# Optimization experiments

Hardware: AMD Instinct MI355X
Metric: run time of the kernel (lower is better)

## Reference

```python
import jax, jax.numpy as jnp
import numpy as np

T = 5          # temporal_window_size
B = 512        # batch (graphs per timestep)
NA = 16        # num_agents (nodes per graph)
S = 64         # num_belief_states
A = 16         # action_dim
HID = 64       # hidden_dim per head
H = 4          # num_attn_heads
FD = HID * H   # 256, feature_dim
LAT = 128      # latent_dim
N = B * NA     # total nodes per timestep
FIN = S + A    # node feature dim
NEG_SLOPE = 0.2


def _edge_index():
    i, j = np.meshgrid(np.arange(NA), np.arange(NA), indexing='ij')
    m = i != j
    src_l, dst_l = i[m], j[m]                      # 240 intra-clique edges
    off = (np.arange(B) * NA)[:, None]
    src = (src_l[None] + off).ravel()
    dst = (dst_l[None] + off).ravel()
    loops = np.arange(N)                           # PyG GATConv add_self_loops=True
    src = np.concatenate([src, loops])
    dst = np.concatenate([dst, loops])
    return jnp.asarray(np.stack([src, dst]), dtype=jnp.int64)


def setup_inputs() -> dict:
    key = jax.random.key(0)
    ks = jax.random.split(key, 24)
    xav = lambda k, shp: jax.random.normal(k, shp, jnp.float32) * np.float32(np.sqrt(2.0 / (shp[0] + shp[-1])))
    return {
        'signals': jax.random.normal(ks[0], (T, B, S), jnp.float32),
        'neighbor_actions': jax.random.normal(ks[1], (T, B, NA * A), jnp.float32),
        'lin_w0': xav(ks[2], (FD, FIN)),
        'att_src0': xav(ks[3], (H, HID)),
        'att_dst0': xav(ks[4], (H, HID)),
        'bias0': jnp.zeros((FD,), jnp.float32),
        'lin_w1': xav(ks[5], (FD, FD)),
        'att_src1': xav(ks[6], (H, HID)),
        'att_dst1': xav(ks[7], (H, HID)),
        'bias1': jnp.zeros((FD,), jnp.float32),
        'in_proj_w': xav(ks[8], (3 * FD, FD)),
        'in_proj_b': jnp.zeros((3 * FD,), jnp.float32),
        'out_proj_w': xav(ks[9], (FD, FD)),
        'out_proj_b': jnp.zeros((FD,), jnp.float32),
        'w_mean': xav(ks[10], (LAT, FD)),
        'b_mean': jnp.zeros((LAT,), jnp.float32),
        'w_logvar': xav(ks[11], (LAT, FD)),
        'b_logvar': jnp.zeros((LAT,), jnp.float32),
        'w_belief': xav(ks[12], (S, FD)),
        'b_belief': jnp.zeros((S,), jnp.float32),
        'edge_index': _edge_index(),
    }


def _segment_softmax(e, seg, num_segments):
    # e: [E, T, H]; softmax over edges sharing the same target node.
    m = jax.ops.segment_max(e, seg, num_segments=num_segments)
    e = jnp.exp(e - m[seg])
    s = jax.ops.segment_sum(e, seg, num_segments=num_segments)
    return e / s[seg]


def _gat(x, src, dst, w, a_src, a_dst, b):
    # x: [N, T, Fin] -> [N, T, H*HID]   (PyG GATConv, concat heads)
    xl = jnp.einsum('ntf,of->nto', x, w).reshape(N, T, H, HID)
    e_src = jnp.einsum('nthc,hc->nth', xl, a_src)[src]   # [E, T, H]
    e_dst = jnp.einsum('nthc,hc->nth', xl, a_dst)[dst]
    e = jax.nn.leaky_relu(e_src + e_dst, NEG_SLOPE)
    alpha = _segment_softmax(e, dst, N)                  # per-target softmax
    out = jax.ops.segment_sum(alpha[..., None] * xl[src], dst, num_segments=N)
    return out.reshape(N, T, FD) + b


def reference(signals, neighbor_actions, lin_w0, att_src0, att_dst0, bias0,
              lin_w1, att_src1, att_dst1, bias1, in_proj_w, in_proj_b,
              out_proj_w, out_proj_b, w_mean, b_mean, w_logvar, b_logvar,
              w_belief, b_belief, edge_index):
    # --- _construct_graph (vectorized over time window + batch) ---
    acts = neighbor_actions.reshape(T, B, NA, A)
    beliefs = jnp.zeros((T, B, NA, S), signals.dtype).at[:, :, 0, :].set(signals)
    nodes = jnp.concatenate([beliefs, acts], -1).reshape(T, N, FIN)
    nodes = jnp.transpose(nodes, (1, 0, 2))              # [N, T, FIN]
    src, dst = edge_index[0], edge_index[1]
    x = jax.nn.relu(_gat(nodes, src, dst, lin_w0, att_src0, att_dst0, bias0))
    x = jax.nn.relu(_gat(x, src, dst, lin_w1, att_src1, att_dst1, bias1))
    # --- ego-node sequence: nodes 0, NA, 2*NA, ... ---
    seq = x[::NA]                                        # [B, T, FD]
    # --- temporal MultiheadAttention (batch_first, eval) ---
    qkv = seq @ in_proj_w.T + in_proj_b
    q, k, v = jnp.split(qkv, 3, axis=-1)
    dh = FD // H
    q = q.reshape(B, T, H, dh); k = k.reshape(B, T, H, dh); v = v.reshape(B, T, H, dh)
    scores = jnp.einsum('bqhd,bkhd->bhqk', q, k) / jnp.sqrt(jnp.asarray(dh, seq.dtype))
    # torch float attn_mask is ADDITIVE: mask[i,j]=1 if j<=i else 0
    mask = (jnp.arange(T)[:, None] >= jnp.arange(T)[None, :]).astype(seq.dtype)
    attn = jax.nn.softmax(scores + mask[None, None], axis=-1)
    ctx = jnp.einsum('bhqk,bkhd->bqhd', attn, v).reshape(B, T, FD)
    ctx = ctx @ out_proj_w.T + out_proj_b
    feat = ctx[:, -1]                                    # [B, FD]
    # --- heads ---
    mean = feat @ w_mean.T + b_mean
    logvar = feat @ w_logvar.T + b_logvar
    belief = jax.nn.softmax(feat @ w_belief.T + b_belief, axis=-1)
    return (mean, logvar, belief)
```

## Files before the change

### kernel.cpp

```cpp
#include <hip/hip_runtime.h>
#include <hip/hip_bf16.h>


__device__ __forceinline__ float wave_sum64(float v) {
    #pragma unroll
    for (int off = 32; off > 0; off >>= 1) v += __shfl_xor(v, off, 64);
    return v;
}
__device__ __forceinline__ float wave_max64(float v) {
    #pragma unroll
    for (int off = 32; off > 0; off >>= 1) v = fmaxf(v, __shfl_xor(v, off, 64));
    return v;
}

__global__ __launch_bounds__(256) void k_pre(
    const float* __restrict__ w0, const float* __restrict__ w1,
    const float* __restrict__ wip, const float* __restrict__ wop,
    const float* __restrict__ wm, const float* __restrict__ wlv,
    const float* __restrict__ wb,
    const float* __restrict__ as0, const float* __restrict__ ad0,
    const float* __restrict__ as1, const float* __restrict__ ad1,
    float* __restrict__ tws,
    float* __restrict__ u1, float* __restrict__ ud1,
    float* __restrict__ pa0, float* __restrict__ pd0)
{
    const int tid = threadIdx.x;
    if (blockIdx.x < 1680) {
        int i = blockIdx.x * 256 + tid;
        float v;
        if (i < 16384) {
            int k = i >> 8, n = i & 255;
            v = w0[n * 80 + k];
        } else if (i < 20480) {
            int j = i - 16384; int k = j >> 8, n = j & 255;
            v = w0[n * 80 + 64 + k];
        } else if (i < 86016) {
            int j = i - 20480; int k = j >> 8, n = j & 255;
            v = w1[n * 256 + k];
        } else if (i < 282624) {
            int j = i - 86016; int k = j / 768, n = j - k * 768;
            v = wip[n * 256 + k];
        } else if (i < 348160) {
            int j = i - 282624; int k = j >> 8, n = j & 255;
            v = wop[n * 256 + k];
        } else {
            int j = i - 348160; int k = j / 320, o = j - k * 320;
            if (o < 128)      v = wm[o * 256 + k];
            else if (o < 256) v = wlv[(o - 128) * 256 + k];
            else              v = wb[(o - 256) * 256 + k];
        }
        tws[i] = v;
        return;
    }
    for (int q = 0; q < 4; q++) {
        int idx = q * 256 + tid;
        int h = idx >> 8, k = idx & 255;
        float su = 0.f, sd = 0.f;
        for (int c = 0; c < 64; c++) {
            float wv = w1[(h * 64 + c) * 256 + k];
            su = fmaf(as1[h * 64 + c], wv, su);
            sd = fmaf(ad1[h * 64 + c], wv, sd);
        }
        u1[idx] = su; ud1[idx] = sd;
    }
    if (tid < 64) {
        int h = tid >> 4, k = tid & 15;
        float su = 0.f, sd = 0.f;
        for (int c = 0; c < 64; c++) {
            float wv = w0[(h * 64 + c) * 80 + 64 + k];
            su = fmaf(as0[h * 64 + c], wv, su);
            sd = fmaf(ad0[h * 64 + c], wv, sd);
        }
        pa0[tid] = su; pd0[tid] = sd;
    }
}

__global__ __launch_bounds__(256, 4) void k_gat(
    const float* __restrict__ sig,
    const float* __restrict__ nact,
    const float* __restrict__ W0sT,
    const float* __restrict__ W0aT,
    const float* __restrict__ W1T,
    const float* __restrict__ u1g, const float* __restrict__ ud1g,
    const float* __restrict__ pa0g, const float* __restrict__ pd0g,
    const float* __restrict__ as0, const float* __restrict__ ad0,
    const float* __restrict__ b0, const float* __restrict__ b1,
    float* __restrict__ seqf)
{
    __shared__ __align__(16) char smem[37120];
    float* actL    = (float*)(smem + 0);
    float* sigL    = (float*)(smem + 1024);
    float* u1L     = (float*)(smem + 1280);
    float* ud1L    = (float*)(smem + 5440);
    float* pa0L    = (float*)(smem + 9600);
    float* pd0L    = (float*)(smem + 9856);
    float* es0w    = (float*)(smem + 10112);
    float* ed0w    = (float*)(smem + 10368);
    float* espL    = (float*)(smem + 10624);
    float* es1L    = (float*)(smem + 11648);
    float* edpL    = (float*)(smem + 11904);
    float* alpha1L = (float*)(smem + 11968);
    float* a0L     = (float*)(smem + 12224);
    float* zL      = (float*)(smem + 16320);
    float* x1L     = (float*)(smem + 20480);

    const int tid = threadIdx.x;
    const int bg = blockIdx.x;
    const int b = bg / 5, g = bg - b * 5;
    const int n = tid, w = tid >> 6, lane = tid & 63;

    if (tid < 64) sigL[tid] = sig[(g * 512 + b) * 64 + tid];
    actL[tid] = nact[(g * 512 + b) * 256 + tid];
    #pragma unroll
    for (int q = 0; q < 4; q++) {
        int idx = q * 256 + tid;
        int h = idx >> 8, k = idx & 255;
        u1L[h * 260 + k] = u1g[idx];
        ud1L[h * 260 + k] = ud1g[idx];
    }
    if (tid >= 64 && tid < 128) {
        pa0L[tid - 64] = pa0g[tid - 64];
        pd0L[tid - 64] = pd0g[tid - 64];
    }
    __syncthreads();

    float S = 0.f;
    {
        const float4* sig4 = (const float4*)sigL;
        #pragma unroll
        for (int i = 0; i < 4; i++) {
            float wv[16];
            #pragma unroll
            for (int j = 0; j < 16; j++)
                wv[j] = W0sT[(i * 16 + j) * 256 + n];
            #pragma unroll
            for (int q = 0; q < 4; q++) {
                float4 sv = sig4[i * 4 + q];
                S = fmaf(wv[q * 4 + 0], sv.x, S);
                S = fmaf(wv[q * 4 + 1], sv.y, S);
                S = fmaf(wv[q * 4 + 2], sv.z, S);
                S = fmaf(wv[q * 4 + 3], sv.w, S);
            }
        }
    }
    const float sS = wave_sum64(S * as0[n]);
    const float dS = wave_sum64(S * ad0[n]);

    if (lane < 16) {
        const int m = lane;
        float su = (m == 0) ? sS : 0.f;
        float sd = (m == 0) ? dS : 0.f;
        const float4* act4 = (const float4*)(actL + m * 16);
        const float4* pa4  = (const float4*)(pa0L + w * 16);
        const float4* pd4  = (const float4*)(pd0L + w * 16);
        #pragma unroll
        for (int q = 0; q < 4; q++) {
            float4 av = act4[q], pv = pa4[q], dv = pd4[q];
            su = fmaf(av.x, pv.x, su); su = fmaf(av.y, pv.y, su);
            su = fmaf(av.z, pv.z, su); su = fmaf(av.w, pv.w, su);
            sd = fmaf(av.x, dv.x, sd); sd = fmaf(av.y, dv.y, sd);
            sd = fmaf(av.z, dv.z, sd); sd = fmaf(av.w, dv.w, sd);
        }
        es0w[w * 16 + m] = su;
        ed0w[w * 16 + m] = sd;
    }
    if (lane < 16) {
        const int j = lane;
        float ej = ed0w[w * 16 + j];
        float e[16], m = -1e30f;
        const float4* es4 = (const float4*)(es0w + w * 16);
        #pragma unroll
        for (int s4 = 0; s4 < 4; s4++) {
            float4 ev = es4[s4];
            float x;
            x = ev.x + ej; x = (x >= 0.f) ? x : 0.2f * x; e[s4*4+0] = x; m = fmaxf(m, x);
            x = ev.y + ej; x = (x >= 0.f) ? x : 0.2f * x; e[s4*4+1] = x; m = fmaxf(m, x);
            x = ev.z + ej; x = (x >= 0.f) ? x : 0.2f * x; e[s4*4+2] = x; m = fmaxf(m, x);
            x = ev.w + ej; x = (x >= 0.f) ? x : 0.2f * x; e[s4*4+3] = x; m = fmaxf(m, x);
        }
        float sum = 0.f;
        #pragma unroll
        for (int s = 0; s < 16; s++) { e[s] = __expf(e[s] - m); sum += e[s]; }
        float inv = 1.f / sum;
        float4* a04 = (float4*)(a0L + w * 256 + j * 16);
        #pragma unroll
        for (int s4 = 0; s4 < 4; s4++)
            a04[s4] = make_float4(e[s4 * 4] * inv, e[s4 * 4 + 1] * inv,
                                  e[s4 * 4 + 2] * inv, e[s4 * 4 + 3] * inv);
    }

    float x1r[16];
    {
        float wr[16];
        #pragma unroll
        for (int k = 0; k < 16; k++) wr[k] = W0aT[k * 256 + n];
        const float4* act4 = (const float4*)actL;
        float xl0r[16];
        #pragma unroll
        for (int s = 0; s < 16; s++) {
            float a = 0.f;
            #pragma unroll
            for (int q = 0; q < 4; q++) {
                float4 av = act4[s * 4 + q];
                a = fmaf(av.x, wr[q * 4 + 0], a);
                a = fmaf(av.y, wr[q * 4 + 1], a);
                a = fmaf(av.z, wr[q * 4 + 2], a);
                a = fmaf(av.w, wr[q * 4 + 3], a);
            }
            xl0r[s] = a;
        }
        xl0r[0] += S;
        const float b0v = b0[n];
        const float4* a04 = (const float4*)(a0L + w * 256);
        #pragma unroll
        for (int j = 0; j < 16; j++) {
            float acc = b0v;
            #pragma unroll
            for (int s4 = 0; s4 < 4; s4++) {
                float4 a4 = a04[j * 4 + s4];
                acc = fmaf(a4.x, xl0r[s4 * 4 + 0], acc);
                acc = fmaf(a4.y, xl0r[s4 * 4 + 1], acc);
                acc = fmaf(a4.z, xl0r[s4 * 4 + 2], acc);
                acc = fmaf(a4.w, xl0r[s4 * 4 + 3], acc);
            }
            x1r[j] = fmaxf(acc, 0.f);
            x1L[j * 260 + n] = x1r[j];
        }
    }
    __syncthreads();

    {
        const int m = tid & 15, h = (tid >> 4) & 3, p = tid >> 6;
        const float4* x4p = (const float4*)(x1L + m * 260 + p * 64);
        const float4* u4p = (const float4*)(u1L + h * 260 + p * 64);
        float a = 0.f;
        #pragma unroll
        for (int i = 0; i < 16; i++) {
            float4 xv = x4p[i], uv = u4p[i];
            a = fmaf(xv.x, uv.x, a);
            a = fmaf(xv.y, uv.y, a);
            a = fmaf(xv.z, uv.z, a);
            a = fmaf(xv.w, uv.w, a);
        }
        espL[m * 16 + h * 4 + p] = a;
        if (m == 0) {
            const float4* ud4p = (const float4*)(ud1L + h * 260 + p * 64);
            float ad = 0.f;
            #pragma unroll
            for (int i = 0; i < 16; i++) {
                float4 xv = x4p[i], uv = ud4p[i];
                ad = fmaf(xv.x, uv.x, ad);
                ad = fmaf(xv.y, uv.y, ad);
                ad = fmaf(xv.z, uv.z, ad);
                ad = fmaf(xv.w, uv.w, ad);
            }
            edpL[h * 4 + p] = ad;
        }
    }
    __syncthreads();

    if (w == 0) {
        {
            const int m = lane >> 2, h = lane & 3;
            const float* e = espL + m * 16 + h * 4;
            es1L[m * 4 + h] = e[0] + e[1] + e[2] + e[3];
        }
        if (lane < 4) {
            const int h = lane;
            float ej = edpL[h * 4] + edpL[h * 4 + 1] + edpL[h * 4 + 2] + edpL[h * 4 + 3];
            float e[16], m = -1e30f;
            #pragma unroll
            for (int s = 0; s < 16; s++) {
                float x = es1L[s * 4 + h] + ej;
                x = (x >= 0.f) ? x : 0.2f * x;
                e[s] = x; m = fmaxf(m, x);
            }
            float sum = 0.f;
            #pragma unroll
            for (int s = 0; s < 16; s++) { e[s] = __expf(e[s] - m); sum += e[s]; }
            float inv = 1.f / sum;
            #pragma unroll
            for (int s = 0; s < 16; s++) alpha1L[h * 16 + s] = e[s] * inv;
        }
    }
    __syncthreads();

    {
        const float4* a14 = (const float4*)alpha1L;
        #pragma unroll
        for (int hh = 0; hh < 4; hh++) {
            float zv = 0.f;
            #pragma unroll
            for (int s4 = 0; s4 < 4; s4++) {
                float4 a4 = a14[hh * 4 + s4];
                zv = fmaf(a4.x, x1r[s4 * 4 + 0], zv);
                zv = fmaf(a4.y, x1r[s4 * 4 + 1], zv);
                zv = fmaf(a4.z, x1r[s4 * 4 + 2], zv);
                zv = fmaf(a4.w, x1r[s4 * 4 + 3], zv);
            }
            zL[hh * 260 + n] = zv;
        }
    }
    __syncthreads();

    {
        const float4* zh = (const float4*)(zL + w * 260);
        float acc = b1[n];
        for (int i = 0; i < 16; i++) {
            float wv[16];
            #pragma unroll
            for (int j = 0; j < 16; j++)
                wv[j] = W1T[(i * 16 + j) * 256 + n];
            #pragma unroll
            for (int q = 0; q < 4; q++) {
                float4 z4 = zh[i * 4 + q];
                acc = fmaf(wv[q * 4 + 0], z4.x, acc);
                acc = fmaf(wv[q * 4 + 1], z4.y, acc);
                acc = fmaf(wv[q * 4 + 2], z4.z, acc);
                acc = fmaf(wv[q * 4 + 3], z4.w, acc);
            }
        }
        seqf[bg * 256 + n] = fmaxf(acc, 0.f);
    }
}

__global__ __launch_bounds__(768) void k_stage2(
    const float* __restrict__ seqf,
    const float* __restrict__ wipT,
    const float* __restrict__ bip,
    const float* __restrict__ wopT,
    const float* __restrict__ bop,
    const float* __restrict__ whT,
    const float* __restrict__ bm, const float* __restrict__ blv,
    const float* __restrict__ bb,
    float* __restrict__ out)
{
    __shared__ float sseq[2][5][256];
    __shared__ float kL[2][5][256], vL[2][5][256], qL[2][256];
    __shared__ float ctxL[2][256], featL[2][256];
    __shared__ float beliefL[2][64];
    const int tid = threadIdx.x;
    const int b0 = blockIdx.x * 2;

    {
        float* sflat = &sseq[0][0][0];
        for (int i = tid; i < 2560; i += 768)
            sflat[i] = seqf[b0 * 1280 + i];
    }
    __syncthreads();

    {
        const int kind = tid >> 8, n = tid & 255;
        if (kind == 0) {
            float a0 = 0.f, a1 = 0.f;
            for (int k = 0; k < 256; k++) {
                float wv = wipT[k * 768 + n];
                a0 = fmaf(sseq[0][4][k], wv, a0);
                a1 = fmaf(sseq[1][4][k], wv, a1);
            }
            float bv = bip[n];
            qL[0][n] = a0 + bv; qL[1][n] = a1 + bv;
        } else {
            const float* wcol = wipT + kind * 256 + n;
            float acc[2][5];
            #pragma unroll
            for (int gb = 0; gb < 2; gb++)
                #pragma unroll
                for (int t = 0; t < 5; t++) acc[gb][t] = 0.f;
            for (int k = 0; k < 256; k++) {
                float wv = wcol[k * 768];
                #pragma unroll
                for (int gb = 0; gb < 2; gb++) {
                    #pragma unroll
                    for (int t = 0; t < 5; t++)
                        acc[gb][t] = fmaf(sseq[gb][t][k], wv, acc[gb][t]);
                }
            }
            float bv = bip[kind * 256 + n];
            float* dst = (kind == 1) ? &kL[0][0][0] : &vL[0][0][0];
            #pragma unroll
            for (int gb = 0; gb < 2; gb++)
                #pragma unroll
                for (int t = 0; t < 5; t++)
                    dst[gb * 1280 + t * 256 + n] = acc[gb][t] + bv;
        }
    }
    __syncthreads();

    if (tid < 512) {
        const int gb = tid >> 8, col = tid & 255;
        float q4 = qL[gb][col];
        float sc[5];
        #pragma unroll
        for (int t = 0; t < 5; t++)
            sc[t] = wave_sum64(q4 * kL[gb][t][col]) * 0.125f;
        float m = sc[0];
        #pragma unroll
        for (int t = 1; t < 5; t++) m = fmaxf(m, sc[t]);
        float p[5], sum = 0.f;
        #pragma unroll
        for (int t = 0; t < 5; t++) { p[t] = __expf(sc[t] - m); sum += p[t]; }
        float inv = 1.f / sum, cv = 0.f;
        #pragma unroll
        for (int t = 0; t < 5; t++) cv = fmaf(p[t], vL[gb][t][col], cv);
        ctxL[gb][col] = cv * inv;
    }
    __syncthreads();

    if (tid < 512) {
        const int gb = tid >> 8, n = tid & 255;
        float acc = 0.f;
        for (int k = 0; k < 256; k++)
            acc = fmaf(ctxL[gb][k], wopT[k * 256 + n], acc);
        featL[gb][n] = acc + bop[n];
    }
    __syncthreads();

    if (tid < 640) {
        const int gb = tid / 320, j = tid - gb * 320;
        float acc = 0.f;
        for (int k = 0; k < 256; k++)
            acc = fmaf(featL[gb][k], whT[k * 320 + j], acc);
        if (j < 128) {
            out[(b0 + gb) * 128 + j] = acc + bm[j];
        } else if (j < 256) {
            out[65536 + (b0 + gb) * 128 + (j - 128)] = acc + blv[j - 128];
        } else {
            beliefL[gb][j - 256] = acc + bb[j - 256];
        }
    }
    __syncthreads();

    if (tid < 128) {
        int gb = tid >> 6, lane = tid & 63;
        float lg = beliefL[gb][lane];
        float m = wave_max64(lg);
        float e = __expf(lg - m);
        float s = wave_sum64(e);
        out[131072 + (b0 + gb) * 64 + lane] = e / s;
    }
}

extern "C" void kernel_launch(void* const* d_in, const int* in_sizes, int n_in,
                              void* d_out, int out_size, void* d_ws, size_t ws_size,
                              hipStream_t stream) {
    const float* sig  = (const float*)d_in[0];
    const float* nact = (const float*)d_in[1];
    const float* w0   = (const float*)d_in[2];
    const float* as0  = (const float*)d_in[3];
    const float* ad0  = (const float*)d_in[4];
    const float* b0   = (const float*)d_in[5];
    const float* w1   = (const float*)d_in[6];
    const float* as1  = (const float*)d_in[7];
    const float* ad1  = (const float*)d_in[8];
    const float* b1   = (const float*)d_in[9];
    const float* wip  = (const float*)d_in[10];
    const float* bip  = (const float*)d_in[11];
    const float* wop  = (const float*)d_in[12];
    const float* bop  = (const float*)d_in[13];
    const float* wm   = (const float*)d_in[14];
    const float* bm   = (const float*)d_in[15];
    const float* wlv  = (const float*)d_in[16];
    const float* blv  = (const float*)d_in[17];
    const float* wb   = (const float*)d_in[18];
    const float* bb   = (const float*)d_in[19];

    float* ws    = (float*)d_ws;
    float* seqf  = ws;
    float* tws   = ws + 655360;
    float* W0sT  = tws;
    float* W0aT  = tws + 16384;
    float* W1T   = tws + 20480;
    float* wipT  = tws + 86016;
    float* wopT  = tws + 282624;
    float* whT   = tws + 348160;
    float* u1    = ws + 1085440;
    float* ud1   = ws + 1086464;
    float* pa0   = ws + 1087488;
    float* pd0   = ws + 1087552;

    k_pre   <<<1681, 256, 0, stream>>>(w0, w1, wip, wop, wm, wlv, wb,
                                       as0, ad0, as1, ad1,
                                       tws, u1, ud1, pa0, pd0);
    k_gat   <<<2560, 256, 0, stream>>>(sig, nact, W0sT, W0aT, W1T,
                                       u1, ud1, pa0, pd0, as0, ad0, b0, b1, seqf);
    k_stage2<<<256, 768, 0, stream>>>(seqf, wipT, bip, wopT, bop, whT,
                                      bm, blv, bb, (float*)d_out);
}
```

Before: 199.8 us.

## Coalesce weight transpose reads, drop u1 LDS staging, simplify GAT weight loops

The weight pre-transpose kernel now reads source matrices contiguously and scatters the transposed writes, where before it gathered strided reads and wrote contiguously. The GAT kernel no longer stages u1/ud1 into shared memory and reads them straight from global memory, which shrinks LDS use. The W0s and W1 matvec loops are changed from explicit 16-register prefetch blocks to partially unrolled loops that read weights inline. The launch-bounds occupancy hint is removed, so register allocation is left to the compiler. Possible downsides are uncoalesced writes in k_pre, repeated global/cache reads of u1, and less memory-level parallelism in the matvec loops.

```diff
diff --git a/kernel.cpp b/kernel.cpp
--- a/kernel.cpp
+++ b/kernel.cpp
@@ -20,36 +20,39 @@
     const float* __restrict__ wb,
     const float* __restrict__ as0, const float* __restrict__ ad0,
     const float* __restrict__ as1, const float* __restrict__ ad1,
-    float* __restrict__ tws,
+    float* __restrict__ W0sT, float* __restrict__ W0aT,
+    float* __restrict__ W1T,  float* __restrict__ wipT,
+    float* __restrict__ wopT, float* __restrict__ whT,
     float* __restrict__ u1, float* __restrict__ ud1,
     float* __restrict__ pa0, float* __restrict__ pd0)
 {
     const int tid = threadIdx.x;
     if (blockIdx.x < 1680) {
         int i = blockIdx.x * 256 + tid;
-        float v;
-        if (i < 16384) {
-            int k = i >> 8, n = i & 255;
-            v = w0[n * 80 + k];
-        } else if (i < 20480) {
-            int j = i - 16384; int k = j >> 8, n = j & 255;
-            v = w0[n * 80 + 64 + k];
+        if (i < 20480) {
+            int n = i / 80, k = i - n * 80;
+            float v = w0[i];
+            if (k < 64) W0sT[k * 256 + n] = v;
+            else        W0aT[(k - 64) * 256 + n] = v;
         } else if (i < 86016) {
-            int j = i - 20480; int k = j >> 8, n = j & 255;
-            v = w1[n * 256 + k];
+            int j = i - 20480; int n = j >> 8, k = j & 255;
+            W1T[k * 256 + n] = w1[j];
         } else if (i < 282624) {
-            int j = i - 86016; int k = j / 768, n = j - k * 768;
-            v = wip[n * 256 + k];
+            int j = i - 86016; int n = j >> 8, k = j & 255;
+            wipT[k * 768 + n] = wip[j];
         } else if (i < 348160) {
-            int j = i - 282624; int k = j >> 8, n = j & 255;
-            v = wop[n * 256 + k];
+            int j = i - 282624; int n = j >> 8, k = j & 255;
+            wopT[k * 256 + n] = wop[j];
+        } else if (i < 380928) {
+            int j = i - 348160; int o = j >> 8, k = j & 255;
+            whT[k * 320 + o] = wm[j];
+        } else if (i < 413696) {
+            int j = i - 380928; int o = j >> 8, k = j & 255;
+            whT[k * 320 + 128 + o] = wlv[j];
         } else {
-            int j = i - 348160; int k = j / 320, o = j - k * 320;
-            if (o < 128)      v = wm[o * 256 + k];
-            else if (o < 256) v = wlv[(o - 128) * 256 + k];
-            else              v = wb[(o - 256) * 256 + k];
-        }
-        tws[i] = v;
+            int j = i - 413696; int o = j >> 8, k = j & 255;
+            whT[k * 320 + 256 + o] = wb[j];
+        }
         return;
     }
     for (int q = 0; q < 4; q++) {
@@ -75,7 +78,7 @@
     }
 }
 
-__global__ __launch_bounds__(256, 4) void k_gat(
+__global__ __launch_bounds__(256) void k_gat(
     const float* __restrict__ sig,
     const float* __restrict__ nact,
     const float* __restrict__ W0sT,
@@ -87,22 +90,20 @@
     const float* __restrict__ b0, const float* __restrict__ b1,
     float* __restrict__ seqf)
 {
-    __shared__ __align__(16) char smem[37120];
+    __shared__ __align__(16) char smem[28800];
     float* actL    = (float*)(smem + 0);
     float* sigL    = (float*)(smem + 1024);
-    float* u1L     = (float*)(smem + 1280);
-    float* ud1L    = (float*)(smem + 5440);
-    float* pa0L    = (float*)(smem + 9600);
-    float* pd0L    = (float*)(smem + 9856);
-    float* es0w    = (float*)(smem + 10112);
-    float* ed0w    = (float*)(smem + 10368);
-    float* espL    = (float*)(smem + 10624);
-    float* es1L    = (float*)(smem + 11648);
-    float* edpL    = (float*)(smem + 11904);
-    float* alpha1L = (float*)(smem + 11968);
-    float* a0L     = (float*)(smem + 12224);
-    float* zL      = (float*)(smem + 16320);
-    float* x1L     = (float*)(smem + 20480);
+    float* pa0L    = (float*)(smem + 1280);
+    float* pd0L    = (float*)(smem + 1536);
+    float* es0w    = (float*)(smem + 1792);
+    float* ed0w    = (float*)(smem + 2048);
+    float* espL    = (float*)(smem + 2304);
+    float* es1L    = (float*)(smem + 3328);
+    float* edpL    = (float*)(smem + 3584);
+    float* alpha1L = (float*)(smem + 3648);
+    float* a0L     = (float*)(smem + 3904);
+    float* zL      = (float*)(smem + 8000);
+    float* x1L     = (float*)(smem + 12160);
 
     const int tid = threadIdx.x;
     const int bg = blockIdx.x;
@@ -111,13 +112,6 @@
 
     if (tid < 64) sigL[tid] = sig[(g * 512 + b) * 64 + tid];
     actL[tid] = nact[(g * 512 + b) * 256 + tid];
-    #pragma unroll
-    for (int q = 0; q < 4; q++) {
-        int idx = q * 256 + tid;
-        int h = idx >> 8, k = idx & 255;
-        u1L[h * 260 + k] = u1g[idx];
-        ud1L[h * 260 + k] = ud1g[idx];
-    }
     if (tid >= 64 && tid < 128) {
         pa0L[tid - 64] = pa0g[tid - 64];
         pd0L[tid - 64] = pd0g[tid - 64];
@@ -127,20 +121,13 @@
     float S = 0.f;
     {
         const float4* sig4 = (const float4*)sigL;
-        #pragma unroll
-        for (int i = 0; i < 4; i++) {
-            float wv[16];
-            #pragma unroll
-            for (int j = 0; j < 16; j++)
-                wv[j] = W0sT[(i * 16 + j) * 256 + n];
-            #pragma unroll
-            for (int q = 0; q < 4; q++) {
-                float4 sv = sig4[i * 4 + q];
-                S = fmaf(wv[q * 4 + 0], sv.x, S);
-                S = fmaf(wv[q * 4 + 1], sv.y, S);
-                S = fmaf(wv[q * 4 + 2], sv.z, S);
-                S = fmaf(wv[q * 4 + 3], sv.w, S);
-            }
+        #pragma unroll 4
+        for (int i = 0; i < 16; i++) {
+            float4 sv = sig4[i];
+            S = fmaf(sv.x, W0sT[(i * 4 + 0) * 256 + n], S);
+            S = fmaf(sv.y, W0sT[(i * 4 + 1) * 256 + n], S);
+            S = fmaf(sv.z, W0sT[(i * 4 + 2) * 256 + n], S);
+            S = fmaf(sv.w, W0sT[(i * 4 + 3) * 256 + n], S);
         }
     }
     const float sS = wave_sum64(S * as0[n]);
@@ -232,7 +219,7 @@
     {
         const int m = tid & 15, h = (tid >> 4) & 3, p = tid >> 6;
         const float4* x4p = (const float4*)(x1L + m * 260 + p * 64);
-        const float4* u4p = (const float4*)(u1L + h * 260 + p * 64);
+        const float4* u4p = (const float4*)(u1g + h * 256 + p * 64);
         float a = 0.f;
         #pragma unroll
         for (int i = 0; i < 16; i++) {
@@ -244,7 +231,7 @@
         }
         espL[m * 16 + h * 4 + p] = a;
         if (m == 0) {
-            const float4* ud4p = (const float4*)(ud1L + h * 260 + p * 64);
+            const float4* ud4p = (const float4*)(ud1g + h * 256 + p * 64);
             float ad = 0.f;
             #pragma unroll
             for (int i = 0; i < 16; i++) {
@@ -306,19 +293,13 @@
     {
         const float4* zh = (const float4*)(zL + w * 260);
         float acc = b1[n];
-        for (int i = 0; i < 16; i++) {
-            float wv[16];
-            #pragma unroll
-            for (int j = 0; j < 16; j++)
-                wv[j] = W1T[(i * 16 + j) * 256 + n];
-            #pragma unroll
-            for (int q = 0; q < 4; q++) {
-                float4 z4 = zh[i * 4 + q];
-                acc = fmaf(wv[q * 4 + 0], z4.x, acc);
-                acc = fmaf(wv[q * 4 + 1], z4.y, acc);
-                acc = fmaf(wv[q * 4 + 2], z4.z, acc);
-                acc = fmaf(wv[q * 4 + 3], z4.w, acc);
-            }
+        #pragma unroll 8
+        for (int i = 0; i < 64; i++) {
+            float4 z4 = zh[i];
+            acc = fmaf(z4.x, W1T[(i * 4 + 0) * 256 + n], acc);
+            acc = fmaf(z4.y, W1T[(i * 4 + 1) * 256 + n], acc);
+            acc = fmaf(z4.z, W1T[(i * 4 + 2) * 256 + n], acc);
+            acc = fmaf(z4.w, W1T[(i * 4 + 3) * 256 + n], acc);
         }
         seqf[bg * 256 + n] = fmaxf(acc, 0.f);
     }
@@ -481,7 +462,8 @@
 
     k_pre   <<<1681, 256, 0, stream>>>(w0, w1, wip, wop, wm, wlv, wb,
                                        as0, ad0, as1, ad1,
-                                       tws, u1, ud1, pa0, pd0);
+                                       W0sT, W0aT, W1T, wipT, wopT, whT,
+                                       u1, ud1, pa0, pd0);
     k_gat   <<<2560, 256, 0, stream>>>(sig, nact, W0sT, W0aT, W1T,
                                        u1, ud1, pa0, pd0, as0, ad0, b0, b1, seqf);
     k_stage2<<<256, 768, 0, stream>>>(seqf, wipT, bip, wopT, bop, whT,
```

After: 209.0 us. +4.6%, slower.
